# Kernel tuning notes

Measured on AMD Instinct MI355X. Metric: run time of the kernel, lower is better.

The kernel has to match this reference:

```python
import jax, jax.numpy as jnp
import numpy as np

EPS = 1e-8
BOX2D_IDX = jnp.array([0, 1, 3, 4, 6])  # x, y, dx, dy, yaw


def box2corners(box):
    # box: (..., 5) = (x, y, w, h, alpha) -> corners (..., 4, 2), CCW order
    x, y, w, h, a = (box[..., i] for i in range(5))
    tx = jnp.array([0.5, -0.5, -0.5, 0.5], box.dtype)
    ty = jnp.array([0.5, 0.5, -0.5, -0.5], box.dtype)
    x4 = tx * w[..., None]
    y4 = ty * h[..., None]
    c, s = jnp.cos(a)[..., None], jnp.sin(a)[..., None]
    rx = c * x4 - s * y4 + x[..., None]
    ry = s * x4 + c * y4 + y[..., None]
    return jnp.stack([rx, ry], axis=-1)


def edge_intersections(c1, c2):
    # all 4x4 edge-edge intersections of two quads -> pts (..., 16, 2), mask (..., 16)
    p1 = c1[..., :, None, :]
    p2 = jnp.roll(c1, -1, axis=-2)[..., :, None, :]
    q1 = c2[..., None, :, :]
    q2 = jnp.roll(c2, -1, axis=-2)[..., None, :, :]
    r = p2 - p1
    s = q2 - q1
    denom = r[..., 0] * s[..., 1] - r[..., 1] * s[..., 0]
    safe = jnp.where(jnp.abs(denom) < EPS, 1.0, denom)
    qp = q1 - p1
    t = (qp[..., 0] * s[..., 1] - qp[..., 1] * s[..., 0]) / safe
    u = (qp[..., 0] * r[..., 1] - qp[..., 1] * r[..., 0]) / safe
    mask = (jnp.abs(denom) > EPS) & (t > 0) & (t < 1) & (u > 0) & (u < 1)
    pts = jnp.where(mask[..., None], p1 + t[..., None] * r, 0.0)
    lead = pts.shape[:-3]
    return pts.reshape(lead + (16, 2)), mask.reshape(lead + (16,))


def points_in_box(pts, corners):
    # pts (..., K, 2) inside rotated quad given by corners (..., 4, 2) -> (..., K) bool
    a = corners[..., 0:1, :]
    ab = corners[..., 1:2, :] - a
    ad = corners[..., 3:4, :] - a
    ap = pts - a
    pab = jnp.sum(ap * ab, -1)
    pad = jnp.sum(ap * ad, -1)
    nab = jnp.sum(ab * ab, -1)
    nad = jnp.sum(ad * ad, -1)
    return (pab > 0) & (pab < nab) & (pad > 0) & (pad < nad)


def masked_polygon_area(verts, mask):
    # verts (..., 24, 2) candidate vertices, mask (..., 24) validity
    m = mask.astype(verts.dtype)
    num = jnp.maximum(jnp.sum(m, -1, keepdims=True), 1.0)
    mean = jnp.sum(verts * m[..., None], -2, keepdims=True) / num[..., None]
    d = verts - mean  # centered (shoelace is translation-invariant)
    ang = jnp.arctan2(d[..., 1], d[..., 0])
    # push invalid vertices to the end with stable tie-break
    ang = jnp.where(mask, ang, 1e6 + jnp.arange(24, dtype=ang.dtype))
    idx = jnp.argsort(ang, axis=-1)
    vs = jnp.take_along_axis(d, idx[..., None], axis=-2)
    ms = jnp.take_along_axis(mask, idx, axis=-1)
    v0 = vs[..., 0:1, :]
    vs = jnp.where(ms[..., None], vs, v0)  # collapse invalid onto first vertex
    nxt = jnp.roll(vs, -1, axis=-2)
    cross = vs[..., 0] * nxt[..., 1] - vs[..., 1] * nxt[..., 0]
    return 0.5 * jnp.abs(jnp.sum(cross, -1))


def rotated_iou_3d(b1, b2):
    # b1, b2: (..., 7) = (x, y, z, dx, dy, dz, yaw); elementwise-aligned IoU
    c1 = box2corners(b1[..., BOX2D_IDX])
    c2 = box2corners(b2[..., BOX2D_IDX])
    ipts, imask = edge_intersections(c1, c2)
    in1 = points_in_box(c1, c2)
    in2 = points_in_box(c2, c1)
    verts = jnp.concatenate([c1, c2, ipts], axis=-2)  # (..., 24, 2)
    mask = jnp.concatenate([in1, in2, imask], axis=-1)
    inter2d = masked_polygon_area(verts, mask)
    zmax = jnp.minimum(b1[..., 2] + 0.5 * b1[..., 5], b2[..., 2] + 0.5 * b2[..., 5])
    zmin = jnp.maximum(b1[..., 2] - 0.5 * b1[..., 5], b2[..., 2] - 0.5 * b2[..., 5])
    inter3d = inter2d * jnp.maximum(zmax - zmin, 0.0)
    v1 = b1[..., 3] * b1[..., 4] * b1[..., 5]
    v2 = b2[..., 3] * b2[..., 4] * b2[..., 5]
    return inter3d / (v1 + v2 - inter3d + EPS)


def setup_inputs() -> dict:
    key = jax.random.key(0)
    k1, k2, k3, k4, k5 = jax.random.split(key, 5)
    N = 1048576
    ctr = (jax.random.uniform(k1, (N, 3)) - 0.5) * 40.0
    dims = jax.random.uniform(k2, (N, 3)) * 2.0 + 0.5
    yaw = (jax.random.uniform(k3, (N, 1)) - 0.5) * (2.0 * np.pi)
    pred = jnp.concatenate([ctr, dims, yaw], axis=-1).astype(jnp.float32)
    noise = jax.random.normal(k4, (N, 7)) * jnp.array(
        [0.3, 0.3, 0.3, 0.2, 0.2, 0.2, 0.2], jnp.float32)
    target = pred + noise
    target = target.at[:, 3:6].set(jnp.maximum(target[:, 3:6], 0.1))
    weight = jax.random.uniform(k5, (N,), dtype=jnp.float32)
    return {"pred": pred, "target": target, "weight": weight}


def reference(pred, target, weight):
    # IoU3DLoss(with_yaw=True, reduction='mean', loss_weight=1.0)
    loss_weight = 1.0
    iou = rotated_iou_3d(pred[None, ...], target[None, ...])  # (1, N)
    iou_loss = (1.0 - iou) * weight
    return loss_weight * jnp.mean(iou_loss)
```

## Files before the change

### kernel.cpp

```cpp
#include <hip/hip_runtime.h>

#define EPS_F 1e-8f
#define BLOCK 256
#define GRID  1024
#define SLAB_CH 896

typedef float vf4 __attribute__((ext_vector_type(4)));

__device__ __forceinline__ vf4 load4u(const float* p) {
    vf4 v;
    __builtin_memcpy(&v, p, 16);
    return v;
}

__device__ __forceinline__ float fast_rcp(float x) {
    return __builtin_amdgcn_rcpf(x);
}

__device__ __forceinline__ void fast_sincos(float x, float* s, float* c) {
    float t = x * 0.15915494309189535f;
    t = __builtin_amdgcn_fractf(t);
    *s = __builtin_amdgcn_sinf(t);
    *c = __builtin_amdgcn_cosf(t);
}

__device__ __forceinline__ float edge_contrib(float ax, float ay,
                                              float dx, float dy,
                                              float rdx, float rdy,
                                              float W, float H) {
    float tA = (-W - ax) * rdx;
    float tB = ( W - ax) * rdx;
    float ta = fmaxf(fminf(tA, tB), 0.f);
    float tb = fminf(fmaxf(tA, tB), 1.f);
    tb = fmaxf(ta, tb);

    float u0 = (-H - ay) * rdy;
    float u1 = ( H - ay) * rdy;
    float tm0 = fminf(u0, u1), tm1 = fmaxf(u0, u1);
    float t1 = fminf(fmaxf(tm0, ta), tb);
    float t2 = fminf(fmaxf(tm1, ta), tb);

    float x0 = fmaf(ta, dx, ax), y0 = fmaf(ta, dy, ay);
    float x1 = fmaf(t1, dx, ax), y1 = fmaf(t1, dy, ay);
    float x2 = fmaf(t2, dx, ax), y2 = fmaf(t2, dy, ay);
    float x3 = fmaf(tb, dx, ax), y3 = fmaf(tb, dy, ay);
    float h0 = fminf(fmaxf(y0, -H), H) + H;
    float h1 = fminf(fmaxf(y1, -H), H) + H;
    float h2 = fminf(fmaxf(y2, -H), H) + H;
    float h3 = fminf(fmaxf(y3, -H), H) + H;

    return (x1 - x0) * (h0 + h1) + (x2 - x1) * (h1 + h2) + (x3 - x2) * (h2 + h3);
}

__global__ __launch_bounds__(BLOCK, 4) void iou3d_partial_kernel(
    const float* __restrict__ pred, const float* __restrict__ target,
    const float* __restrict__ weight, float* __restrict__ partials,
    int N, int stride_e, int iters)
{
    __shared__ vf4 lds4[2 * SLAB_CH];
    const int tid = threadIdx.x;
    const long maxdw = 7L * N - 4;


    {
        long g0 = (long)blockIdx.x * 256 * 7;
        #pragma unroll
        for (int k = 0; k < 4; ++k) {
            int c = k * BLOCK + tid;
            if (c < SLAB_CH) {
                bool isP = (c < 448);
                long gdw = g0 + 4L * c - (isP ? 0 : 1792);
                gdw = (gdw > maxdw) ? maxdw : gdw;
                lds4[c] = load4u((isP ? pred : target) + gdw);
            }
        }
    }
    int i0 = blockIdx.x * 256 + tid;
    float wcur = (i0 < N) ? weight[i0] : 0.f;
    __syncthreads();

    float val = 0.f;
    #pragma unroll 1
    for (int it = 0; it < iters; ++it) {
        bool more = (it + 1 < iters);

        vf4 R0, R1, R2, R3;
        float wnext = 0.f;
        if (more) {
            long g0 = ((long)blockIdx.x * 256 + (long)(it + 1) * stride_e) * 7;
            {
                int c = tid;              long g = g0 + 4L * c;
                g = (g > maxdw) ? maxdw : g;  R0 = load4u(pred + g);
            }
            {
                int c = BLOCK + tid;      long g = g0 + 4L * c;
                g = (g > maxdw) ? maxdw : g;  R1 = load4u(pred + g);
            }
            {
                int c = 2 * BLOCK + tid;  long g = g0 + 4L * c - 1792;
                g = (g > maxdw) ? maxdw : g;  R2 = load4u(target + g);
            }
            {
                int c = 3 * BLOCK + tid;
                long g = g0 + 4L * c - 1792;
                g = (g < 0) ? 0 : ((g > maxdw) ? maxdw : g);
                R3 = load4u(target + g);
            }
            int inext = blockIdx.x * 256 + (it + 1) * stride_e + tid;
            wnext = (inext < N) ? weight[inext] : 0.f;
        }

        if (more) {
            int c = BLOCK + tid;
            if (c >= 448) {
                long g0 = ((long)blockIdx.x * 256 + (long)(it + 1) * stride_e) * 7;
                long g = g0 + 4L * c - 1792;
                g = (g > maxdw) ? maxdw : g;
                R1 = load4u(target + g);
            }
        }

        {
            const float* ldsf = (const float*)(lds4 + (it & 1) * 0);
            const float* base = (const float*)lds4;
            const float* p;
            const float* q;
            p = base + (size_t)(it & 1) * (SLAB_CH * 4) + 7 * tid;
            q = p + 1792;
            (void)ldsf;

            float a0 = p[0], a1 = p[1], a2 = p[2], a3 = p[3], a4 = p[4], a5 = p[5], a6 = p[6];
            float b0 = q[0], b1 = q[1], b2 = q[2], b3 = q[3], b4 = q[4], b5 = q[5], b6 = q[6];

            float s1, c1, sd, cd;
            fast_sincos(a6, &s1, &c1);
            fast_sincos(b6 - a6, &sd, &cd);
            float dxc = b0 - a0, dyc = b1 - a1;
            float tx =  c1 * dxc + s1 * dyc;
            float ty = -s1 * dxc + c1 * dyc;
            float W = 0.5f * a3, H = 0.5f * a4;
            float w2 = 0.5f * b3, h2 = 0.5f * b4;

            float cw = cd * w2, sw = sd * w2, ch = cd * h2, sh = sd * h2;
            float q0x =  cw - sh + tx, q0y =  sw + ch + ty;
            float q1x = -cw - sh + tx, q1y = -sw + ch + ty;
            float q2x = -cw + sh + tx, q2y = -sw - ch + ty;
            float q3x =  cw + sh + tx, q3y =  sw - ch + ty;

            float e0x = -2.f * cw, e0y = -2.f * sw;
            float e1x =  2.f * sh, e1y = -2.f * ch;
            float g0x = (fabsf(e0x) < 1e-20f) ? 1e-20f : e0x;
            float g0y = (fabsf(e0y) < 1e-20f) ? 1e-20f : e0y;
            float g1x = (fabsf(e1x) < 1e-20f) ? 1e-20f : e1x;
            float g1y = (fabsf(e1y) < 1e-20f) ? 1e-20f : e1y;
            float r0x = fast_rcp(g0x), r0y = fast_rcp(g0y);
            float r1x = fast_rcp(g1x), r1y = fast_rcp(g1y);

            float s = edge_contrib(q0x, q0y,  e0x,  e0y,  r0x,  r0y, W, H)
                    + edge_contrib(q1x, q1y,  e1x,  e1y,  r1x,  r1y, W, H)
                    + edge_contrib(q2x, q2y, -e0x, -e0y, -r0x, -r0y, W, H)
                    + edge_contrib(q3x, q3y, -e1x, -e1y, -r1x, -r1y, W, H);
            float area = 0.5f * fabsf(s);

            float zmax = fminf(a2 + 0.5f * a5, b2 + 0.5f * b5);
            float zmin = fmaxf(a2 - 0.5f * a5, b2 - 0.5f * b5);
            float inter3d = area * fmaxf(zmax - zmin, 0.f);
            float v1 = a3 * a4 * a5;
            float v2 = b3 * b4 * b5;
            float iou = inter3d * fast_rcp(v1 + v2 - inter3d + EPS_F);
            val += (1.f - iou) * wcur;
        }

        if (more) {
            vf4* dst = lds4 + ((it + 1) & 1) * SLAB_CH;
            dst[tid]             = R0;
            dst[BLOCK + tid]     = R1;
            dst[2 * BLOCK + tid] = R2;
            if (3 * BLOCK + tid < SLAB_CH) dst[3 * BLOCK + tid] = R3;
        }
        __syncthreads();
        wcur = wnext;
    }

    #pragma unroll
    for (int off = 32; off > 0; off >>= 1) val += __shfl_down(val, off, 64);
    __shared__ float wsum[4];
    int lane = tid & 63, wid = tid >> 6;
    if (lane == 0) wsum[wid] = val;
    __syncthreads();
    if (tid == 0)
        partials[blockIdx.x] = wsum[0] + wsum[1] + wsum[2] + wsum[3];
}

__global__ __launch_bounds__(BLOCK) void reduce_partials_kernel(
    const float* __restrict__ partials, float* __restrict__ out,
    int nparts, float invN)
{
    float v = 0.f;
    for (int k = threadIdx.x; k < nparts; k += BLOCK) v += partials[k];
    #pragma unroll
    for (int off = 32; off > 0; off >>= 1) v += __shfl_down(v, off, 64);
    __shared__ float wsum[4];
    int lane = threadIdx.x & 63, wid = threadIdx.x >> 6;
    if (lane == 0) wsum[wid] = v;
    __syncthreads();
    if (threadIdx.x == 0)
        out[0] = (wsum[0] + wsum[1] + wsum[2] + wsum[3]) * invN;
}

extern "C" void kernel_launch(void* const* d_in, const int* in_sizes, int n_in,
                              void* d_out, int out_size, void* d_ws, size_t ws_size,
                              hipStream_t stream) {
    const float* pred   = (const float*)d_in[0];
    const float* target = (const float*)d_in[1];
    const float* weight = (const float*)d_in[2];
    float* out = (float*)d_out;
    float* partials = (float*)d_ws;
    int N = in_sizes[2];

    int nblocks = (N + BLOCK - 1) / BLOCK;
    int grid = (nblocks < GRID) ? nblocks : GRID;
    int stride_e = grid * BLOCK;
    int iters = (N + stride_e - 1) / stride_e;

    iou3d_partial_kernel<<<grid, BLOCK, 0, stream>>>(pred, target, weight,
                                                     partials, N, stride_e, iters);
    reduce_partials_kernel<<<1, BLOCK, 0, stream>>>(partials, out, grid,
                                                    1.f / (float)N);
}
```

Baseline: 98.42 us.

## Stage input slabs via direct global-to-LDS loads and drop bounds clamping

The main kernel now copies each block's pred/target slab straight into LDS with the amdgcn global_load_lds builtin. This replaces the register round-trip and explicit LDS stores, and removes the per-load bounds clamps when N divides the grid stride evenly. The aim is to cut VGPR pressure and extra instructions in the double-buffered prefetch. A fallback kernel that loads records directly from global memory handles N values that do not divide evenly. The risk is whether the async LDS loads are correctly ordered by the existing barrier before the data is consumed.

```diff
diff --git a/kernel.cpp b/kernel.cpp
--- a/kernel.cpp
+++ b/kernel.cpp
@@ -4,19 +4,19 @@
 #define BLOCK 256
 #define GRID  1024
 #define SLAB_CH 896
+#define SLAB_DW (SLAB_CH * 4)
 
 typedef float vf4 __attribute__((ext_vector_type(4)));
 
+typedef const __attribute__((address_space(1))) void* gptr_t;
+typedef __attribute__((address_space(3))) void* sptr_t;
+
 __device__ __forceinline__ vf4 load4u(const float* p) {
-    vf4 v;
-    __builtin_memcpy(&v, p, 16);
-    return v;
-}
-
+    vf4 v; __builtin_memcpy(&v, p, 16); return v;
+}
 __device__ __forceinline__ float fast_rcp(float x) {
     return __builtin_amdgcn_rcpf(x);
 }
-
 __device__ __forceinline__ void fast_sincos(float x, float* s, float* c) {
     float t = x * 0.15915494309189535f;
     t = __builtin_amdgcn_fractf(t);
@@ -52,134 +52,95 @@
     return (x1 - x0) * (h0 + h1) + (x2 - x1) * (h1 + h2) + (x3 - x2) * (h2 + h3);
 }
 
-__global__ __launch_bounds__(BLOCK, 4) void iou3d_partial_kernel(
+__device__ __forceinline__ float elem_loss(const float* p, const float* q,
+                                           float wgt) {
+    float a0=p[0],a1=p[1],a2=p[2],a3=p[3],a4=p[4],a5=p[5],a6=p[6];
+    float b0=q[0],b1=q[1],b2=q[2],b3=q[3],b4=q[4],b5=q[5],b6=q[6];
+
+    float s1, c1, sd, cd;
+    fast_sincos(a6, &s1, &c1);
+    fast_sincos(b6 - a6, &sd, &cd);
+    float dxc = b0 - a0, dyc = b1 - a1;
+    float tx =  c1 * dxc + s1 * dyc;
+    float ty = -s1 * dxc + c1 * dyc;
+    float W = 0.5f * a3, H = 0.5f * a4;
+    float w2 = 0.5f * b3, h2 = 0.5f * b4;
+
+    float cw = cd * w2, sw = sd * w2, ch = cd * h2, sh = sd * h2;
+    float q0x =  cw - sh + tx, q0y =  sw + ch + ty;
+    float q1x = -cw - sh + tx, q1y = -sw + ch + ty;
+    float q2x = -cw + sh + tx, q2y = -sw - ch + ty;
+    float q3x =  cw + sh + tx, q3y =  sw - ch + ty;
+
+    float e0x = -2.f * cw, e0y = -2.f * sw;
+    float e1x =  2.f * sh, e1y = -2.f * ch;
+    float g0x = (fabsf(e0x) < 1e-20f) ? 1e-20f : e0x;
+    float g0y = (fabsf(e0y) < 1e-20f) ? 1e-20f : e0y;
+    float g1x = (fabsf(e1x) < 1e-20f) ? 1e-20f : e1x;
+    float g1y = (fabsf(e1y) < 1e-20f) ? 1e-20f : e1y;
+    float r0x = fast_rcp(g0x), r0y = fast_rcp(g0y);
+    float r1x = fast_rcp(g1x), r1y = fast_rcp(g1y);
+
+    float s = edge_contrib(q0x, q0y,  e0x,  e0y,  r0x,  r0y, W, H)
+            + edge_contrib(q1x, q1y,  e1x,  e1y,  r1x,  r1y, W, H)
+            + edge_contrib(q2x, q2y, -e0x, -e0y, -r0x, -r0y, W, H)
+            + edge_contrib(q3x, q3y, -e1x, -e1y, -r1x, -r1y, W, H);
+    float area = 0.5f * fabsf(s);
+
+    float zmax = fminf(a2 + 0.5f * a5, b2 + 0.5f * b5);
+    float zmin = fmaxf(a2 - 0.5f * a5, b2 - 0.5f * b5);
+    float inter3d = area * fmaxf(zmax - zmin, 0.f);
+    float v1 = a3 * a4 * a5;
+    float v2 = b3 * b4 * b5;
+    float iou = inter3d * fast_rcp(v1 + v2 - inter3d + EPS_F);
+    return (1.f - iou) * wgt;
+}
+
+__global__ __launch_bounds__(BLOCK, 4) void iou3d_partial_dma(
     const float* __restrict__ pred, const float* __restrict__ target,
     const float* __restrict__ weight, float* __restrict__ partials,
-    int N, int stride_e, int iters)
+    int stride_e, int iters)
 {
     __shared__ vf4 lds4[2 * SLAB_CH];
     const int tid = threadIdx.x;
-    const long maxdw = 7L * N - 4;
-
-
-    {
-        long g0 = (long)blockIdx.x * 256 * 7;
+
+    auto stage = [&](int it, int buf) {
+        long g0 = ((long)blockIdx.x * BLOCK + (long)it * stride_e) * 7;
         #pragma unroll
-        for (int k = 0; k < 4; ++k) {
+        for (int k = 0; k < 3; ++k) {
             int c = k * BLOCK + tid;
-            if (c < SLAB_CH) {
-                bool isP = (c < 448);
-                long gdw = g0 + 4L * c - (isP ? 0 : 1792);
-                gdw = (gdw > maxdw) ? maxdw : gdw;
-                lds4[c] = load4u((isP ? pred : target) + gdw);
-            }
+            const float* src = (c < 448) ? pred + g0 + 4L * c
+                                         : target + g0 + 4L * c - SLAB_DW / 2;
+            __builtin_amdgcn_global_load_lds((gptr_t)src,
+                                             (sptr_t)&lds4[buf * SLAB_CH + c],
+                                             16, 0, 0);
         }
-    }
-    int i0 = blockIdx.x * 256 + tid;
-    float wcur = (i0 < N) ? weight[i0] : 0.f;
+        if (tid < 128) {
+            int c = 3 * BLOCK + tid;
+            const float* src = target + g0 + 4L * c - SLAB_DW / 2;
+            __builtin_amdgcn_global_load_lds((gptr_t)src,
+                                             (sptr_t)&lds4[buf * SLAB_CH + c],
+                                             16, 0, 0);
+        }
+    };
+
+    stage(0, 0);
+    int i0 = blockIdx.x * BLOCK + tid;
+    float wcur = weight[i0];
     __syncthreads();
 
     float val = 0.f;
     #pragma unroll 1
     for (int it = 0; it < iters; ++it) {
         bool more = (it + 1 < iters);
-
-        vf4 R0, R1, R2, R3;
-        float wnext = 0.f;
-        if (more) {
-            long g0 = ((long)blockIdx.x * 256 + (long)(it + 1) * stride_e) * 7;
-            {
-                int c = tid;              long g = g0 + 4L * c;
-                g = (g > maxdw) ? maxdw : g;  R0 = load4u(pred + g);
-            }
-            {
-                int c = BLOCK + tid;      long g = g0 + 4L * c;
-                g = (g > maxdw) ? maxdw : g;  R1 = load4u(pred + g);
-            }
-            {
-                int c = 2 * BLOCK + tid;  long g = g0 + 4L * c - 1792;
-                g = (g > maxdw) ? maxdw : g;  R2 = load4u(target + g);
-            }
-            {
-                int c = 3 * BLOCK + tid;
-                long g = g0 + 4L * c - 1792;
-                g = (g < 0) ? 0 : ((g > maxdw) ? maxdw : g);
-                R3 = load4u(target + g);
-            }
-            int inext = blockIdx.x * 256 + (it + 1) * stride_e + tid;
-            wnext = (inext < N) ? weight[inext] : 0.f;
-        }
-
-        if (more) {
-            int c = BLOCK + tid;
-            if (c >= 448) {
-                long g0 = ((long)blockIdx.x * 256 + (long)(it + 1) * stride_e) * 7;
-                long g = g0 + 4L * c - 1792;
-                g = (g > maxdw) ? maxdw : g;
-                R1 = load4u(target + g);
-            }
-        }
-
-        {
-            const float* ldsf = (const float*)(lds4 + (it & 1) * 0);
-            const float* base = (const float*)lds4;
-            const float* p;
-            const float* q;
-            p = base + (size_t)(it & 1) * (SLAB_CH * 4) + 7 * tid;
-            q = p + 1792;
-            (void)ldsf;
-
-            float a0 = p[0], a1 = p[1], a2 = p[2], a3 = p[3], a4 = p[4], a5 = p[5], a6 = p[6];
-            float b0 = q[0], b1 = q[1], b2 = q[2], b3 = q[3], b4 = q[4], b5 = q[5], b6 = q[6];
-
-            float s1, c1, sd, cd;
-            fast_sincos(a6, &s1, &c1);
-            fast_sincos(b6 - a6, &sd, &cd);
-            float dxc = b0 - a0, dyc = b1 - a1;
-            float tx =  c1 * dxc + s1 * dyc;
-            float ty = -s1 * dxc + c1 * dyc;
-            float W = 0.5f * a3, H = 0.5f * a4;
-            float w2 = 0.5f * b3, h2 = 0.5f * b4;
-
-            float cw = cd * w2, sw = sd * w2, ch = cd * h2, sh = sd * h2;
-            float q0x =  cw - sh + tx, q0y =  sw + ch + ty;
-            float q1x = -cw - sh + tx, q1y = -sw + ch + ty;
-            float q2x = -cw + sh + tx, q2y = -sw - ch + ty;
-            float q3x =  cw + sh + tx, q3y =  sw - ch + ty;
-
-            float e0x = -2.f * cw, e0y = -2.f * sw;
-            float e1x =  2.f * sh, e1y = -2.f * ch;
-            float g0x = (fabsf(e0x) < 1e-20f) ? 1e-20f : e0x;
-            float g0y = (fabsf(e0y) < 1e-20f) ? 1e-20f : e0y;
-            float g1x = (fabsf(e1x) < 1e-20f) ? 1e-20f : e1x;
-            float g1y = (fabsf(e1y) < 1e-20f) ? 1e-20f : e1y;
-            float r0x = fast_rcp(g0x), r0y = fast_rcp(g0y);
-            float r1x = fast_rcp(g1x), r1y = fast_rcp(g1y);
-
-            float s = edge_contrib(q0x, q0y,  e0x,  e0y,  r0x,  r0y, W, H)
-                    + edge_contrib(q1x, q1y,  e1x,  e1y,  r1x,  r1y, W, H)
-                    + edge_contrib(q2x, q2y, -e0x, -e0y, -r0x, -r0y, W, H)
-                    + edge_contrib(q3x, q3y, -e1x, -e1y, -r1x, -r1y, W, H);
-            float area = 0.5f * fabsf(s);
-
-            float zmax = fminf(a2 + 0.5f * a5, b2 + 0.5f * b5);
-            float zmin = fmaxf(a2 - 0.5f * a5, b2 - 0.5f * b5);
-            float inter3d = area * fmaxf(zmax - zmin, 0.f);
-            float v1 = a3 * a4 * a5;
-            float v2 = b3 * b4 * b5;
-            float iou = inter3d * fast_rcp(v1 + v2 - inter3d + EPS_F);
-            val += (1.f - iou) * wcur;
-        }
-
-        if (more) {
-            vf4* dst = lds4 + ((it + 1) & 1) * SLAB_CH;
-            dst[tid]             = R0;
-            dst[BLOCK + tid]     = R1;
-            dst[2 * BLOCK + tid] = R2;
-            if (3 * BLOCK + tid < SLAB_CH) dst[3 * BLOCK + tid] = R3;
-        }
+        if (more) stage(it + 1, (it + 1) & 1);
+        float wnext = more ? weight[i0 + (it + 1) * stride_e] : 0.f;
+
+        const float* base = (const float*)lds4 + (size_t)(it & 1) * SLAB_DW;
+        val += elem_loss(base + 7 * tid, base + SLAB_DW / 2 + 7 * tid, wcur);
+
+        wcur = wnext;
         __syncthreads();
-        wcur = wnext;
     }
 
     #pragma unroll
@@ -189,6 +150,47 @@
     if (lane == 0) wsum[wid] = val;
     __syncthreads();
     if (tid == 0)
+        partials[blockIdx.x] = wsum[0] + wsum[1] + wsum[2] + wsum[3];
+}
+
+__global__ __launch_bounds__(BLOCK, 4) void iou3d_partial_gen(
+    const float* __restrict__ pred, const float* __restrict__ target,
+    const float* __restrict__ weight, float* __restrict__ partials,
+    int N, int stride_e, int iters)
+{
+    int i = blockIdx.x * BLOCK + threadIdx.x;
+    int j = (i < N) ? i : 0;
+    long o = (long)j * 7;
+    vf4 A0 = load4u(pred + o),  A1 = load4u(pred + o + 3);
+    vf4 B0 = load4u(target + o), B1 = load4u(target + o + 3);
+    float wg = (i < N) ? weight[j] : 0.f;
+
+    float val = 0.f;
+    #pragma unroll 1
+    for (int it = 0; it < iters; ++it) {
+        vf4 a0 = A0, a1 = A1, b0 = B0, b1 = B1;
+        float w = wg;
+        int inext = i + stride_e;
+        if (it + 1 < iters) {
+            int jn = (inext < N) ? inext : 0;
+            long on = (long)jn * 7;
+            A0 = load4u(pred + on);  A1 = load4u(pred + on + 3);
+            B0 = load4u(target + on); B1 = load4u(target + on + 3);
+            wg = (inext < N) ? weight[jn] : 0.f;
+        }
+        i = inext;
+        float rec[14] = {a0.x,a0.y,a0.z,a0.w,a1.y,a1.z,a1.w,
+                         b0.x,b0.y,b0.z,b0.w,b1.y,b1.z,b1.w};
+        val += elem_loss(rec, rec + 7, w);
+    }
+
+    #pragma unroll
+    for (int off = 32; off > 0; off >>= 1) val += __shfl_down(val, off, 64);
+    __shared__ float wsum[4];
+    int lane = threadIdx.x & 63, wid = threadIdx.x >> 6;
+    if (lane == 0) wsum[wid] = val;
+    __syncthreads();
+    if (threadIdx.x == 0)
         partials[blockIdx.x] = wsum[0] + wsum[1] + wsum[2] + wsum[3];
 }
 
@@ -223,8 +225,13 @@
     int stride_e = grid * BLOCK;
     int iters = (N + stride_e - 1) / stride_e;
 
-    iou3d_partial_kernel<<<grid, BLOCK, 0, stream>>>(pred, target, weight,
-                                                     partials, N, stride_e, iters);
+    if (N % stride_e == 0) {
+        iou3d_partial_dma<<<grid, BLOCK, 0, stream>>>(pred, target, weight,
+                                                      partials, stride_e, iters);
+    } else {
+        iou3d_partial_gen<<<grid, BLOCK, 0, stream>>>(pred, target, weight,
+                                                      partials, N, stride_e, iters);
+    }
     reduce_partials_kernel<<<1, BLOCK, 0, stream>>>(partials, out, grid,
                                                     1.f / (float)N);
 }
```

Result: faster. 95.23 us (-3.2%).
